# Kernel optimization log

Hardware: AMD Instinct MI355X
Metric: run time of the kernel (lower is better)

## Reference

```python
import jax, jax.numpy as jnp
import numpy as np

N = 50000      # nodes
E = 800000     # edges
IN_DIM = 128
HID = 16       # per-head hidden dim (layer1)
HEADS = 8
OUT_DIM = 32   # layer2 output dim (1 head)
NEG_SLOPE = 0.2  # GAT-paper LeakyReLU slope


def _gat_layer(x, W, a_src, a_dst, src, dst, num_nodes):
    """One multi-head GAT layer.
    x: [N, Fin]; W: [Fin, H*D]; a_src/a_dst: [H, D]; src/dst: [E].
    Returns [N, H, D].
    """
    H, D = a_src.shape
    z = (x @ W).reshape(num_nodes, H, D)            # [N, H, D]
    # edge attention logits: attn_fc([z_src || z_dst]) split into two dots
    e_s = jnp.einsum('nhd,hd->nh', z, a_src)        # [N, H]
    e_d = jnp.einsum('nhd,hd->nh', z, a_dst)        # [N, H]
    e = e_s[src] + e_d[dst]                          # [E, H]
    e = jnp.where(e >= 0, e, NEG_SLOPE * e)          # leaky_relu
    # softmax over incoming edges of each destination node
    m = jax.ops.segment_max(e, dst, num_segments=num_nodes)   # [N, H]
    ex = jnp.exp(e - m[dst])                                   # [E, H]
    s = jax.ops.segment_sum(ex, dst, num_segments=num_nodes)  # [N, H]
    alpha = ex / s[dst]                                        # [E, H]
    msg = alpha[:, :, None] * z[src]                            # [E, H, D]
    return jax.ops.segment_sum(msg, dst, num_segments=num_nodes)  # [N, H, D]


def setup_inputs() -> dict:
    key = jax.random.key(0)
    ks = jax.random.split(key, 9)
    h = jax.random.normal(ks[0], (N, IN_DIM), dtype=jnp.float32)
    src = jax.random.randint(ks[1], (E,), 0, N, dtype=jnp.int32)
    dst = jax.random.randint(ks[2], (E,), 0, N, dtype=jnp.int32)
    sc1 = 1.0 / np.sqrt(IN_DIM)
    W1 = jax.random.normal(ks[3], (IN_DIM, HEADS * HID), dtype=jnp.float32) * sc1
    a1_src = jax.random.normal(ks[4], (HEADS, HID), dtype=jnp.float32) * 0.1
    a1_dst = jax.random.normal(ks[5], (HEADS, HID), dtype=jnp.float32) * 0.1
    sc2 = 1.0 / np.sqrt(HEADS * HID)
    W2 = jax.random.normal(ks[6], (HEADS * HID, OUT_DIM), dtype=jnp.float32) * sc2
    a2_src = jax.random.normal(ks[7], (1, OUT_DIM), dtype=jnp.float32) * 0.1
    a2_dst = jax.random.normal(ks[8], (1, OUT_DIM), dtype=jnp.float32) * 0.1
    return {"h": h, "W1": W1, "a1_src": a1_src, "a1_dst": a1_dst,
            "W2": W2, "a2_src": a2_src, "a2_dst": a2_dst,
            "src": src, "dst": dst}


def reference(h, W1, a1_src, a1_dst, W2, a2_src, a2_dst, src, dst):
    # layer1: multi-head, concat heads -> [N, HEADS*HID]
    h1 = _gat_layer(h, W1, a1_src, a1_dst, src, dst, N).reshape(N, HEADS * HID)
    h1 = jax.nn.elu(h1)
    # layer2: single head -> [N, OUT_DIM]
    out = _gat_layer(h1, W2, a2_src, a2_dst, src, dst, N).reshape(N, OUT_DIM)
    return out
```

## Files before the change

### kernel.cpp

```cpp
#include <hip/hip_runtime.h>
#include <hip/hip_fp16.h>
#include <math.h>

#define NN 50000
#define EE 800000
#define FIN 128
#define F1  128
#define NH  8
#define DH  16
#define F2  32
#define SLOPE 0.2f
#define LOG2E 1.44269504f

#define EB 4096
#define NBLK ((EE + EB - 1) / EB)
#define HB 2048
#define NHBLK ((EE + HB - 1) / HB)
#define BK  391
#define SEGCAP 4096
#define PREPB 80
#define GEMM1B ((NN + 63) / 64)
#define ATT1B  (BK * 8)
#define GEMM2B ((NN + 63) / 64)
#define CHUNK 2560

typedef _Float16 f16x8 __attribute__((ext_vector_type(8)));
typedef float    f32x4 __attribute__((ext_vector_type(4)));

__global__ __launch_bounds__(256) void k1_hist_prep(const int* __restrict__ dst,
        const float* __restrict__ W1, const float* __restrict__ W2,
        __half* __restrict__ wt1, __half* __restrict__ wt2, int* __restrict__ hist) {
    int tid = threadIdx.x;
    if (blockIdx.x < NHBLK) {
        __shared__ int lc[BK];
        for (int i = tid; i < BK; i += 256) lc[i] = 0;
        __syncthreads();
        int base = blockIdx.x * HB;
        int end = base + HB; if (end > EE) end = EE;
        for (int i = base + tid; i < end; i += 256)
            atomicAdd(&lc[dst[i] >> 7], 1);
        __syncthreads();
        for (int i = tid; i < BK; i += 256)
            if (lc[i]) atomicAdd(&hist[i], lc[i]);
    } else {
        int gidx = (blockIdx.x - NHBLK) * 256 + tid;
        if (gidx < FIN * F1) {
            int n = gidx >> 7, k = gidx & 127;
            wt1[gidx] = __float2half(W1[k * F1 + n]);
        } else {
            int t2 = gidx - FIN * F1;
            if (t2 < F2 * FIN) {
                int n = t2 >> 7, k = t2 & 127;
                wt2[t2] = __float2half(W2[k * F2 + n]);
            }
        }
    }
}

extern __shared__ char smem_k2[];
__global__ __launch_bounds__(256) void k2_split_gemm1(const int* __restrict__ src,
        const int* __restrict__ dst, const int* __restrict__ hist, int* __restrict__ cursor,
        unsigned int* __restrict__ sorted,
        const float* __restrict__ h, const __half* __restrict__ wt1,
        const float* __restrict__ a1s, const float* __restrict__ a1d,
        __half* __restrict__ z1s, float* __restrict__ es1x, float* __restrict__ ed1x) {
    int tid = threadIdx.x;
    if (blockIdx.x < NBLK) {
        unsigned int*   recs = (unsigned int*)smem_k2;
        unsigned short* rbk  = (unsigned short*)(smem_k2 + 16384);
        int* lc    = (int*)(smem_k2 + 24576);
        int* lofs  = (int*)(smem_k2 + 26624);
        int* lcur  = (int*)(smem_k2 + 28672);
        int* delta = (int*)(smem_k2 + 30720);
        int* bscan = (int*)(smem_k2 + 32768);
        int* sh    = (int*)(smem_k2 + 34816);
        for (int i = tid; i < 512; i += 256) lc[i] = 0;
        __syncthreads();
        int base = blockIdx.x * EB;
        int cnt = EE - base; if (cnt > EB) cnt = EB;
        unsigned int myrec[16];
        #pragma unroll
        for (int k = 0; k < 16; ++k) {
            int i = base + tid + k * 256;
            myrec[k] = 0xFFFFFFFFu;
            if (i - base < cnt) {
                unsigned int d = (unsigned int)dst[i];
                myrec[k] = (d << 16) | (unsigned int)src[i];
                atomicAdd(&lc[d >> 7], 1);
            }
        }
        __syncthreads();
        int a0 = lc[2 * tid], a1 = lc[2 * tid + 1];
        int tsum = a0 + a1;
        sh[tid] = tsum;
        __syncthreads();
        for (int off = 1; off < 256; off <<= 1) {
            int t = (tid >= off) ? sh[tid - off] : 0;
            __syncthreads(); sh[tid] += t; __syncthreads();
        }
        int ex = sh[tid] - tsum;
        lofs[2 * tid] = ex;
        lofs[2 * tid + 1] = ex + a0;
        __syncthreads();
        int h0 = hist[2 * tid], h1 = hist[2 * tid + 1];
        int hsum = h0 + h1;
        sh[tid] = hsum;
        __syncthreads();
        for (int off = 1; off < 256; off <<= 1) {
            int t = (tid >= off) ? sh[tid - off] : 0;
            __syncthreads(); sh[tid] += t; __syncthreads();
        }
        int hex = sh[tid] - hsum;
        bscan[2 * tid] = hex;
        bscan[2 * tid + 1] = hex + h0;
        __syncthreads();
        for (int b = tid; b < BK; b += 256) {
            int c = lc[b];
            lcur[b] = lofs[b];
            if (c) {
                int g = atomicAdd(&cursor[b], c);
                delta[b] = bscan[b] + g - lofs[b];
            }
        }
        __syncthreads();
        #pragma unroll
        for (int k = 0; k < 16; ++k) {
            if (myrec[k] != 0xFFFFFFFFu) {
                int b = (int)(myrec[k] >> 23);
                int pos = atomicAdd(&lcur[b], 1);
                recs[pos] = myrec[k];
                rbk[pos] = (unsigned short)b;
            }
        }
        __syncthreads();
        for (int s = tid; s < cnt; s += 256)
            sorted[s + delta[rbk[s]]] = recs[s];
    } else {
        __half* hs  = (__half*)smem_k2;
        __half* wls = (__half*)(smem_k2 + 17408);
        for (int c = tid; c < 2048; c += 256) {
            int row = c >> 4, ch = c & 15;
            *(float4*)&wls[row * 136 + ch * 8] = *(const float4*)&wt1[row * 128 + ch * 8];
        }
        int rowBase = (blockIdx.x - NBLK) * 64;
        for (int idx4 = tid; idx4 < 64 * 32; idx4 += 256) {
            int r = idx4 >> 5, cc = (idx4 & 31) * 4;
            int n = rowBase + r;
            float4 v = (n < NN) ? *(const float4*)&h[(size_t)n * FIN + cc] : make_float4(0, 0, 0, 0);
            union { __half2 h2[2]; int2 i; } u;
            u.h2[0] = __floats2half2_rn(v.x, v.y);
            u.h2[1] = __floats2half2_rn(v.z, v.w);
            *(int2*)&hs[r * 136 + cc] = u.i;
        }
        __syncthreads();
        int l = tid & 63, w = tid >> 6;
        int q = l >> 4, cl = l & 15;
        int m0 = w * 16;
        float as[8], ad[8];
        #pragma unroll
        for (int t = 0; t < 8; ++t) { as[t] = a1s[t * DH + cl]; ad[t] = a1d[t * DH + cl]; }
        f32x4 acc[8];
        #pragma unroll
        for (int t = 0; t < 8; ++t) acc[t] = (f32x4){0.f, 0.f, 0.f, 0.f};
        const __half* ap = &hs[(m0 + cl) * 136 + q * 8];
        const __half* bp = &wls[cl * 136 + q * 8];
        #pragma unroll
        for (int k0 = 0; k0 < 128; k0 += 32) {
            f16x8 af = *(const f16x8*)(ap + k0);
            #pragma unroll
            for (int t = 0; t < 8; ++t) {
                f16x8 bf = *(const f16x8*)(bp + t * 16 * 136 + k0);
                acc[t] = __builtin_amdgcn_mfma_f32_16x16x32_f16(af, bf, acc[t], 0, 0, 0);
            }
        }
        #pragma unroll
        for (int t = 0; t < 8; ++t) {
            #pragma unroll
            for (int reg = 0; reg < 4; ++reg) {
                int row = rowBase + m0 + q * 4 + reg;
                float z = acc[t][reg];
                float s = z * as[t], d = z * ad[t];
                s += __shfl_xor(s, 1, 64); d += __shfl_xor(d, 1, 64);
                s += __shfl_xor(s, 2, 64); d += __shfl_xor(d, 2, 64);
                s += __shfl_xor(s, 4, 64); d += __shfl_xor(d, 4, 64);
                s += __shfl_xor(s, 8, 64); d += __shfl_xor(d, 8, 64);
                if (row < NN) {
                    z1s[(size_t)t * (NN * 16) + (size_t)row * 16 + cl] = __float2half(z);
                    if (cl == 0) {
                        es1x[row * NH + t] = s * LOG2E;
                        ed1x[row * NH + t] = d * LOG2E;
                    }
                }
            }
        }
    }
}

__global__ __launch_bounds__(256) void csrbuild_kernel(const int* __restrict__ hist,
        const unsigned int* __restrict__ sorted, unsigned short* __restrict__ csr,
        const float* __restrict__ es1x, const float* __restrict__ ed1x,
        float* __restrict__ w1p, int* __restrict__ row_ptr) {
    __shared__ unsigned int recs[SEGCAP];
    __shared__ unsigned short csr_sh[SEGCAP];
    __shared__ unsigned char dst_sh[SEGCAP];
    __shared__ float ed_sh[128 * NH];
    __shared__ int ncnt[128], ncur[128];
    __shared__ int sh[256];
    __shared__ int bscan[512];
    int b = blockIdx.x;
    int tid = threadIdx.x;
    int h0 = hist[2 * tid], h1 = hist[2 * tid + 1];
    int hsum = h0 + h1;
    sh[tid] = hsum;
    if (tid < 128) ncnt[tid] = 0;
    for (int idx = tid; idx < 128 * NH; idx += 256) {
        int node = b * 128 + (idx >> 3);
        ed_sh[idx] = (node < NN) ? ed1x[node * NH + (idx & 7)] : 0.f;
    }
    __syncthreads();
    for (int off = 1; off < 256; off <<= 1) {
        int t = (tid >= off) ? sh[tid - off] : 0;
        __syncthreads(); sh[tid] += t; __syncthreads();
    }
    int hex = sh[tid] - hsum;
    bscan[2 * tid] = hex;
    bscan[2 * tid + 1] = hex + h0;
    __syncthreads();
    int s0 = bscan[b], s1 = bscan[b + 1];
    int cnt = s1 - s0; if (cnt > SEGCAP) cnt = SEGCAP;
    for (int i = tid; i < cnt; i += 256) {
        unsigned int r = sorted[s0 + i];
        recs[i] = r;
        atomicAdd(&ncnt[(r >> 16) & 127], 1);
    }
    __syncthreads();
    int v = (tid < 128) ? ncnt[tid] : 0;
    sh[tid] = v;
    __syncthreads();
    for (int off = 1; off < 256; off <<= 1) {
        int t = (tid >= off) ? sh[tid - off] : 0;
        __syncthreads(); sh[tid] += t; __syncthreads();
    }
    int ex = sh[tid] - v;
    if (tid < 128) {
        ncur[tid] = ex;
        int node = b * 128 + tid;
        if (node < NN) row_ptr[node] = s0 + ex;
    }
    if (b == BK - 1 && tid == 0) row_ptr[NN] = EE;
    __syncthreads();
    for (int i = tid; i < cnt; i += 256) {
        unsigned int r = recs[i];
        int local = (r >> 16) & 127;
        int p = atomicAdd(&ncur[local], 1);
        csr_sh[p] = (unsigned short)(r & 0xFFFFu);
        dst_sh[p] = (unsigned char)local;
    }
    __syncthreads();
    for (int i = tid; i < cnt; i += 256) {
        unsigned short sv = csr_sh[i];
        unsigned char lv = dst_sh[i];
        csr[s0 + i] = sv;
        float4 ea = *(const float4*)&es1x[(size_t)sv * NH];
        float4 eb = *(const float4*)&es1x[(size_t)sv * NH + 4];
        float es8[8] = {ea.x, ea.y, ea.z, ea.w, eb.x, eb.y, eb.z, eb.w};
        const float* edp = &ed_sh[(int)lv * NH];
        #pragma unroll
        for (int hh = 0; hh < 8; ++hh) {
            float e = es8[hh] + edp[hh];
            e = e >= 0.f ? e : SLOPE * e;
            w1p[(size_t)hh * EE + s0 + i] = exp2f(e);
        }
    }
}

__global__ __launch_bounds__(256, 8) void attn1_slice_kernel(const int* __restrict__ row_ptr,
        const unsigned short* __restrict__ csr, const __half* __restrict__ z1s,
        const float* __restrict__ w1p, __half* __restrict__ h1s) {
    __shared__ unsigned short csr_sh[CHUNK];
    __shared__ float w_sh[CHUNK];
    int hl = blockIdx.x & 7;
    int tile = blockIdx.x >> 3;
    int nodeBase = tile * 128;
    int tid = threadIdx.x;
    int n = nodeBase + (tid >> 1);
    int j = tid & 1;
    const __half* zp = z1s + (size_t)hl * (NN * 16) + j * 8;
    const float* wp = w1p + (size_t)hl * EE;
    int tBeg = row_ptr[nodeBase];
    int nEnd = nodeBase + 128; if (nEnd > NN) nEnd = NN;
    int tEnd = row_ptr[nEnd];
    int b0 = 0, b1 = -1;
    if (n < NN) { b0 = row_ptr[n]; b1 = row_ptr[n + 1]; }
    float acc[8] = {0.f, 0.f, 0.f, 0.f, 0.f, 0.f, 0.f, 0.f};
    float ws = 0.f;
    for (int c0 = tBeg; c0 < tEnd; c0 += CHUNK) {
        int c1 = c0 + CHUNK; if (c1 > tEnd) c1 = tEnd;
        for (int i = c0 + tid; i < c1; i += 256) {
            csr_sh[i - c0] = csr[i];
            w_sh[i - c0] = wp[i];
        }
        __syncthreads();
        int lo = b0 > c0 ? b0 : c0;
        int hi = b1 < c1 ? b1 : c1;
        int i = lo;
        for (; i + 4 <= hi; i += 4) {
            int r = i - c0;
            int s0 = csr_sh[r], s1 = csr_sh[r + 1], s2 = csr_sh[r + 2], s3 = csr_sh[r + 3];
            float w0 = w_sh[r], w1 = w_sh[r + 1], w2 = w_sh[r + 2], w3 = w_sh[r + 3];
            union { float4 f; __half2 h2[4]; } u0, u1, u2, u3;
            u0.f = *(const float4*)&zp[(size_t)s0 * 16];
            u1.f = *(const float4*)&zp[(size_t)s1 * 16];
            u2.f = *(const float4*)&zp[(size_t)s2 * 16];
            u3.f = *(const float4*)&zp[(size_t)s3 * 16];
            ws += (w0 + w1) + (w2 + w3);
            #pragma unroll
            for (int t = 0; t < 4; ++t) {
                float2 v0 = __half22float2(u0.h2[t]);
                float2 v1 = __half22float2(u1.h2[t]);
                float2 v2 = __half22float2(u2.h2[t]);
                float2 v3 = __half22float2(u3.h2[t]);
                acc[2*t]   = fmaf(w0, v0.x, fmaf(w1, v1.x, fmaf(w2, v2.x, fmaf(w3, v3.x, acc[2*t]))));
                acc[2*t+1] = fmaf(w0, v0.y, fmaf(w1, v1.y, fmaf(w2, v2.y, fmaf(w3, v3.y, acc[2*t+1]))));
            }
        }
        for (; i < hi; ++i) {
            int r = i - c0;
            int s = csr_sh[r];
            float wv = w_sh[r];
            ws += wv;
            union { float4 f; __half2 h2[4]; } u;
            u.f = *(const float4*)&zp[(size_t)s * 16];
            #pragma unroll
            for (int t = 0; t < 4; ++t) {
                float2 v = __half22float2(u.h2[t]);
                acc[2*t]   = fmaf(wv, v.x, acc[2*t]);
                acc[2*t+1] = fmaf(wv, v.y, acc[2*t+1]);
            }
        }
        __syncthreads();
    }
    if (n < NN) {
        float rs = ws > 0.f ? 1.0f / ws : 0.f;
        union { float4 f; __half2 h2[4]; } p;
        #pragma unroll
        for (int t = 0; t < 4; ++t) {
            float x0 = acc[2*t] * rs, x1 = acc[2*t+1] * rs;
            x0 = x0 > 0.f ? x0 : __expf(x0) - 1.0f;
            x1 = x1 > 0.f ? x1 : __expf(x1) - 1.0f;
            p.h2[t] = __floats2half2_rn(x0, x1);
        }
        *(float4*)&h1s[(size_t)hl * (NN * 16) + (size_t)n * 16 + j * 8] = p.f;
    }
}

__global__ __launch_bounds__(256) void gemm2_kernel(const __half* __restrict__ h1s,
        const __half* __restrict__ wt2, const float* __restrict__ a2s, const float* __restrict__ a2d,
        __half* __restrict__ z2h, float* __restrict__ es2x, float* __restrict__ ed2x) {
    __shared__ alignas(16) __half hs[64 * 136];
    __shared__ alignas(16) __half wls[32 * 136];
    int tid = threadIdx.x;
    for (int c = tid; c < 512; c += 256) {
        int row = c >> 4, ch = c & 15;
        *(float4*)&wls[row * 136 + ch * 8] = *(const float4*)&wt2[row * 128 + ch * 8];
    }
    int rowBase = blockIdx.x * 64;
    for (int idx = tid; idx < 1024; idx += 256) {
        int j2 = idx & 1, nl = (idx >> 1) & 63, pl = idx >> 7;
        int n = rowBase + nl;
        float4 v = (n < NN) ? *(const float4*)&h1s[(size_t)pl * (NN * 16) + (size_t)n * 16 + j2 * 8]
                            : make_float4(0, 0, 0, 0);
        *(float4*)&hs[nl * 136 + pl * 16 + j2 * 8] = v;
    }
    __syncthreads();
    int l = tid & 63, w = tid >> 6;
    int q = l >> 4, cl = l & 15;
    int m0 = w * 16;
    float as0 = a2s[cl], as1 = a2s[16 + cl];
    float ad0 = a2d[cl], ad1 = a2d[16 + cl];
    f32x4 acc2[2];
    acc2[0] = (f32x4){0.f, 0.f, 0.f, 0.f};
    acc2[1] = (f32x4){0.f, 0.f, 0.f, 0.f};
    const __half* ap = &hs[(m0 + cl) * 136 + q * 8];
    const __half* bp = &wls[cl * 136 + q * 8];
    #pragma unroll
    for (int k0 = 0; k0 < 128; k0 += 32) {
        f16x8 af = *(const f16x8*)(ap + k0);
        #pragma unroll
        for (int t = 0; t < 2; ++t) {
            f16x8 bf = *(const f16x8*)(bp + t * 16 * 136 + k0);
            acc2[t] = __builtin_amdgcn_mfma_f32_16x16x32_f16(af, bf, acc2[t], 0, 0, 0);
        }
    }
    #pragma unroll
    for (int reg = 0; reg < 4; ++reg) {
        int row = rowBase + m0 + q * 4 + reg;
        float s = acc2[0][reg] * as0 + acc2[1][reg] * as1;
        float d = acc2[0][reg] * ad0 + acc2[1][reg] * ad1;
        s += __shfl_xor(s, 1, 64); d += __shfl_xor(d, 1, 64);
        s += __shfl_xor(s, 2, 64); d += __shfl_xor(d, 2, 64);
        s += __shfl_xor(s, 4, 64); d += __shfl_xor(d, 4, 64);
        s += __shfl_xor(s, 8, 64); d += __shfl_xor(d, 8, 64);
        if (row < NN) {
            z2h[(size_t)row * F2 + cl]      = __float2half(acc2[0][reg]);
            z2h[(size_t)row * F2 + 16 + cl] = __float2half(acc2[1][reg]);
            if (cl == 0) {
                es2x[row] = s * LOG2E;
                ed2x[row] = d * LOG2E;
            }
        }
    }
}

__global__ __launch_bounds__(128) void attn2_kernel(const int* __restrict__ row_ptr,
        const unsigned short* __restrict__ csr, const __half* __restrict__ z2h,
        const float* __restrict__ es, const float* __restrict__ ed,
        float* __restrict__ out) {
    int gt = blockIdx.x * 128 + threadIdx.x;
    int n = gt >> 3;
    int j = gt & 7;
    if (n >= NN) return;
    int b0 = row_ptr[n];
    int cnt = row_ptr[n + 1] - b0;
    float edn = ed[n];
    float acc[4] = {0.f, 0.f, 0.f, 0.f};
    float ws = 0.f;
    int i = 0;
    for (; i + 4 <= cnt; i += 4) {
        int s0 = csr[b0 + i], s1 = csr[b0 + i + 1], s2 = csr[b0 + i + 2], s3 = csr[b0 + i + 3];
        float e0 = es[s0] + edn;
        float e1 = es[s1] + edn;
        float e2 = es[s2] + edn;
        float e3 = es[s3] + edn;
        union { float2 f; __half2 h2[2]; } u0, u1, u2, u3;
        u0.f = *(const float2*)&z2h[(size_t)s0 * F2 + j * 4];
        u1.f = *(const float2*)&z2h[(size_t)s1 * F2 + j * 4];
        u2.f = *(const float2*)&z2h[(size_t)s2 * F2 + j * 4];
        u3.f = *(const float2*)&z2h[(size_t)s3 * F2 + j * 4];
        float w0 = exp2f(e0 >= 0.f ? e0 : SLOPE * e0);
        float w1 = exp2f(e1 >= 0.f ? e1 : SLOPE * e1);
        float w2 = exp2f(e2 >= 0.f ? e2 : SLOPE * e2);
        float w3 = exp2f(e3 >= 0.f ? e3 : SLOPE * e3);
        ws += (w0 + w1) + (w2 + w3);
        #pragma unroll
        for (int t = 0; t < 2; ++t) {
            float2 v0 = __half22float2(u0.h2[t]);
            float2 v1 = __half22float2(u1.h2[t]);
            float2 v2 = __half22float2(u2.h2[t]);
            float2 v3 = __half22float2(u3.h2[t]);
            acc[2*t]   = fmaf(w0, v0.x, fmaf(w1, v1.x, fmaf(w2, v2.x, fmaf(w3, v3.x, acc[2*t]))));
            acc[2*t+1] = fmaf(w0, v0.y, fmaf(w1, v1.y, fmaf(w2, v2.y, fmaf(w3, v3.y, acc[2*t+1]))));
        }
    }
    for (; i < cnt; ++i) {
        int s = csr[b0 + i];
        float e = es[s] + edn;
        float wv = exp2f(e >= 0.f ? e : SLOPE * e);
        ws += wv;
        union { float2 f; __half2 h2[2]; } u;
        u.f = *(const float2*)&z2h[(size_t)s * F2 + j * 4];
        #pragma unroll
        for (int t = 0; t < 2; ++t) {
            float2 v = __half22float2(u.h2[t]);
            acc[2*t]   = fmaf(wv, v.x, acc[2*t]);
            acc[2*t+1] = fmaf(wv, v.y, acc[2*t+1]);
        }
    }
    float rs = ws > 0.f ? 1.0f / ws : 0.f;
    *(float4*)&out[(size_t)n * F2 + j * 4] =
        make_float4(acc[0]*rs, acc[1]*rs, acc[2]*rs, acc[3]*rs);
}

extern "C" void kernel_launch(void* const* d_in, const int* in_sizes, int n_in,
                              void* d_out, int out_size, void* d_ws, size_t ws_size,
                              hipStream_t stream) {
    const float* h   = (const float*)d_in[0];
    const float* W1  = (const float*)d_in[1];
    const float* a1s = (const float*)d_in[2];
    const float* a1d = (const float*)d_in[3];
    const float* W2  = (const float*)d_in[4];
    const float* a2s = (const float*)d_in[5];
    const float* a2d = (const float*)d_in[6];
    const int*   src = (const int*)d_in[7];
    const int*   dst = (const int*)d_in[8];
    float* out = (float*)d_out;

    int* ip      = (int*)d_ws;
    int* hist    = ip;
    int* cursor  = hist + 512;
    int* row_ptr = cursor + 512;
    unsigned int* sorted = (unsigned int*)(row_ptr + NN + 8);
    unsigned short* csr16 = (unsigned short*)(sorted + EE);
    float* es1x = (float*)(csr16 + EE);
    float* ed1x = es1x + (size_t)NN * NH;
    float* es2x = ed1x + (size_t)NN * NH;
    float* ed2x = es2x + NN;
    __half* z1s = (__half*)(ed2x + NN);
    __half* z2h = z1s + (size_t)NN * F1;
    __half* wt1 = z2h + (size_t)NN * F2;
    __half* wt2 = wt1 + FIN * F1;
    __half* h1s = wt2 + F2 * FIN;
    float* w1p  = (float*)(h1s + (size_t)NN * F1);

    hipMemsetAsync(hist, 0, 1024 * sizeof(int), stream);

    k1_hist_prep<<<NHBLK + PREPB, 256, 0, stream>>>(dst, W1, W2, wt1, wt2, hist);
    k2_split_gemm1<<<NBLK + GEMM1B, 256, 52224, stream>>>(src, dst, hist, cursor, sorted,
                                                          h, wt1, a1s, a1d, z1s, es1x, ed1x);
    csrbuild_kernel<<<BK, 256, 0, stream>>>(hist, sorted, csr16, es1x, ed1x, w1p, row_ptr);
    attn1_slice_kernel<<<ATT1B, 256, 0, stream>>>(row_ptr, csr16, z1s, w1p, h1s);
    gemm2_kernel<<<GEMM2B, 256, 0, stream>>>(h1s, wt2, a2s, a2d, z2h, es2x, ed2x);
    attn2_kernel<<<(NN * 8 + 127) / 128, 128, 0, stream>>>(row_ptr, csr16, z2h, es2x, ed2x, out);
}
```

Baseline: 200.6 us.

## Stage attn2 edge tiles in shared memory and unroll attn1 gather by eight

attn2 is restructured so each 256-thread block handles 64 nodes: it cooperatively loads the block's contiguous CSR range and the gathered source logits into shared memory, then each thread accumulates two nodes from LDS instead of reading the CSR indices and es values redundantly per 8-lane group. attn1 gains an 8-way unrolled gather loop with occupancy hint lowered from 8 to 4 waves to allow more registers, giving more memory-level parallelism. This costs more register pressure and extra block-wide syncs, and each thread now serially handles two nodes.

```diff
diff --git a/kernel.cpp b/kernel.cpp
--- a/kernel.cpp
+++ b/kernel.cpp
@@ -23,6 +23,8 @@
 #define ATT1B  (BK * 8)
 #define GEMM2B ((NN + 63) / 64)
 #define CHUNK 2560
+#define ATT2B ((NN + 63) / 64)
+#define CHUNK2 1536
 
 typedef _Float16 f16x8 __attribute__((ext_vector_type(8)));
 typedef float    f32x4 __attribute__((ext_vector_type(4)));
@@ -274,7 +276,7 @@
     }
 }
 
-__global__ __launch_bounds__(256, 8) void attn1_slice_kernel(const int* __restrict__ row_ptr,
+__global__ __launch_bounds__(256, 4) void attn1_slice_kernel(const int* __restrict__ row_ptr,
         const unsigned short* __restrict__ csr, const __half* __restrict__ z1s,
         const float* __restrict__ w1p, __half* __restrict__ h1s) {
     __shared__ unsigned short csr_sh[CHUNK];
@@ -304,6 +306,38 @@
         int lo = b0 > c0 ? b0 : c0;
         int hi = b1 < c1 ? b1 : c1;
         int i = lo;
+        for (; i + 8 <= hi; i += 8) {
+            int r = i - c0;
+            int s0 = csr_sh[r],     s1 = csr_sh[r + 1], s2 = csr_sh[r + 2], s3 = csr_sh[r + 3];
+            int s4 = csr_sh[r + 4], s5 = csr_sh[r + 5], s6 = csr_sh[r + 6], s7 = csr_sh[r + 7];
+            float w0 = w_sh[r],     w1 = w_sh[r + 1], w2 = w_sh[r + 2], w3 = w_sh[r + 3];
+            float w4 = w_sh[r + 4], w5 = w_sh[r + 5], w6 = w_sh[r + 6], w7 = w_sh[r + 7];
+            union { float4 f; __half2 h2[4]; } u0, u1, u2, u3, u4, u5, u6, u7;
+            u0.f = *(const float4*)&zp[(size_t)s0 * 16];
+            u1.f = *(const float4*)&zp[(size_t)s1 * 16];
+            u2.f = *(const float4*)&zp[(size_t)s2 * 16];
+            u3.f = *(const float4*)&zp[(size_t)s3 * 16];
+            u4.f = *(const float4*)&zp[(size_t)s4 * 16];
+            u5.f = *(const float4*)&zp[(size_t)s5 * 16];
+            u6.f = *(const float4*)&zp[(size_t)s6 * 16];
+            u7.f = *(const float4*)&zp[(size_t)s7 * 16];
+            ws += ((w0 + w1) + (w2 + w3)) + ((w4 + w5) + (w6 + w7));
+            #pragma unroll
+            for (int t = 0; t < 4; ++t) {
+                float2 v0 = __half22float2(u0.h2[t]);
+                float2 v1 = __half22float2(u1.h2[t]);
+                float2 v2 = __half22float2(u2.h2[t]);
+                float2 v3 = __half22float2(u3.h2[t]);
+                float2 v4 = __half22float2(u4.h2[t]);
+                float2 v5 = __half22float2(u5.h2[t]);
+                float2 v6 = __half22float2(u6.h2[t]);
+                float2 v7 = __half22float2(u7.h2[t]);
+                acc[2*t]   = fmaf(w0, v0.x, fmaf(w1, v1.x, fmaf(w2, v2.x, fmaf(w3, v3.x, acc[2*t]))));
+                acc[2*t]   = fmaf(w4, v4.x, fmaf(w5, v5.x, fmaf(w6, v6.x, fmaf(w7, v7.x, acc[2*t]))));
+                acc[2*t+1] = fmaf(w0, v0.y, fmaf(w1, v1.y, fmaf(w2, v2.y, fmaf(w3, v3.y, acc[2*t+1]))));
+                acc[2*t+1] = fmaf(w4, v4.y, fmaf(w5, v5.y, fmaf(w6, v6.y, fmaf(w7, v7.y, acc[2*t+1]))));
+            }
+        }
         for (; i + 4 <= hi; i += 4) {
             int r = i - c0;
             int s0 = csr_sh[r], s1 = csr_sh[r + 1], s2 = csr_sh[r + 2], s3 = csr_sh[r + 3];
@@ -412,63 +446,98 @@
     }
 }
 
-__global__ __launch_bounds__(128) void attn2_kernel(const int* __restrict__ row_ptr,
+__global__ __launch_bounds__(256) void attn2_kernel(const int* __restrict__ row_ptr,
         const unsigned short* __restrict__ csr, const __half* __restrict__ z2h,
         const float* __restrict__ es, const float* __restrict__ ed,
         float* __restrict__ out) {
-    int gt = blockIdx.x * 128 + threadIdx.x;
-    int n = gt >> 3;
-    int j = gt & 7;
-    if (n >= NN) return;
-    int b0 = row_ptr[n];
-    int cnt = row_ptr[n + 1] - b0;
-    float edn = ed[n];
-    float acc[4] = {0.f, 0.f, 0.f, 0.f};
-    float ws = 0.f;
-    int i = 0;
-    for (; i + 4 <= cnt; i += 4) {
-        int s0 = csr[b0 + i], s1 = csr[b0 + i + 1], s2 = csr[b0 + i + 2], s3 = csr[b0 + i + 3];
-        float e0 = es[s0] + edn;
-        float e1 = es[s1] + edn;
-        float e2 = es[s2] + edn;
-        float e3 = es[s3] + edn;
-        union { float2 f; __half2 h2[2]; } u0, u1, u2, u3;
-        u0.f = *(const float2*)&z2h[(size_t)s0 * F2 + j * 4];
-        u1.f = *(const float2*)&z2h[(size_t)s1 * F2 + j * 4];
-        u2.f = *(const float2*)&z2h[(size_t)s2 * F2 + j * 4];
-        u3.f = *(const float2*)&z2h[(size_t)s3 * F2 + j * 4];
-        float w0 = exp2f(e0 >= 0.f ? e0 : SLOPE * e0);
-        float w1 = exp2f(e1 >= 0.f ? e1 : SLOPE * e1);
-        float w2 = exp2f(e2 >= 0.f ? e2 : SLOPE * e2);
-        float w3 = exp2f(e3 >= 0.f ? e3 : SLOPE * e3);
-        ws += (w0 + w1) + (w2 + w3);
-        #pragma unroll
-        for (int t = 0; t < 2; ++t) {
-            float2 v0 = __half22float2(u0.h2[t]);
-            float2 v1 = __half22float2(u1.h2[t]);
-            float2 v2 = __half22float2(u2.h2[t]);
-            float2 v3 = __half22float2(u3.h2[t]);
-            acc[2*t]   = fmaf(w0, v0.x, fmaf(w1, v1.x, fmaf(w2, v2.x, fmaf(w3, v3.x, acc[2*t]))));
-            acc[2*t+1] = fmaf(w0, v0.y, fmaf(w1, v1.y, fmaf(w2, v2.y, fmaf(w3, v3.y, acc[2*t+1]))));
-        }
-    }
-    for (; i < cnt; ++i) {
-        int s = csr[b0 + i];
-        float e = es[s] + edn;
-        float wv = exp2f(e >= 0.f ? e : SLOPE * e);
-        ws += wv;
-        union { float2 f; __half2 h2[2]; } u;
-        u.f = *(const float2*)&z2h[(size_t)s * F2 + j * 4];
-        #pragma unroll
-        for (int t = 0; t < 2; ++t) {
-            float2 v = __half22float2(u.h2[t]);
-            acc[2*t]   = fmaf(wv, v.x, acc[2*t]);
-            acc[2*t+1] = fmaf(wv, v.y, acc[2*t+1]);
-        }
-    }
-    float rs = ws > 0.f ? 1.0f / ws : 0.f;
-    *(float4*)&out[(size_t)n * F2 + j * 4] =
-        make_float4(acc[0]*rs, acc[1]*rs, acc[2]*rs, acc[3]*rs);
+    __shared__ unsigned short csr_sh[CHUNK2];
+    __shared__ float es_sh[CHUNK2];
+    int nodeBase = blockIdx.x * 64;
+    int tid = threadIdx.x;
+    int j = tid & 7;
+    int na = nodeBase + (tid >> 3);
+    int nb = na + 32;
+    int tBeg = row_ptr[nodeBase];
+    int nEnd = nodeBase + 64; if (nEnd > NN) nEnd = NN;
+    int tEnd = row_ptr[nEnd];
+    int b0a = 0, b1a = -1, b0b = 0, b1b = -1;
+    float edA = 0.f, edB = 0.f;
+    if (na < NN) { b0a = row_ptr[na]; b1a = row_ptr[na + 1]; edA = ed[na]; }
+    if (nb < NN) { b0b = row_ptr[nb]; b1b = row_ptr[nb + 1]; edB = ed[nb]; }
+    float accA[4] = {0.f, 0.f, 0.f, 0.f}, accB[4] = {0.f, 0.f, 0.f, 0.f};
+    float wsA = 0.f, wsB = 0.f;
+    for (int c0 = tBeg; c0 < tEnd; c0 += CHUNK2) {
+        int c1 = c0 + CHUNK2; if (c1 > tEnd) c1 = tEnd;
+        for (int i = c0 + tid; i < c1; i += 256) {
+            unsigned short s = csr[i];
+            csr_sh[i - c0] = s;
+            es_sh[i - c0] = es[s];
+        }
+        __syncthreads();
+        #pragma unroll
+        for (int half = 0; half < 2; ++half) {
+            int lo = (half ? b0b : b0a), hi = (half ? b1b : b1a);
+            float edn = half ? edB : edA;
+            float* acc = half ? accB : accA;
+            float& wsr = half ? wsB : wsA;
+            if (lo < c0) lo = c0;
+            if (hi > c1) hi = c1;
+            int i = lo;
+            for (; i + 4 <= hi; i += 4) {
+                int r = i - c0;
+                int s0 = csr_sh[r], s1 = csr_sh[r + 1], s2 = csr_sh[r + 2], s3 = csr_sh[r + 3];
+                float e0 = es_sh[r] + edn;
+                float e1 = es_sh[r + 1] + edn;
+                float e2 = es_sh[r + 2] + edn;
+                float e3 = es_sh[r + 3] + edn;
+                union { float2 f; __half2 h2[2]; } u0, u1, u2, u3;
+                u0.f = *(const float2*)&z2h[(size_t)s0 * F2 + j * 4];
+                u1.f = *(const float2*)&z2h[(size_t)s1 * F2 + j * 4];
+                u2.f = *(const float2*)&z2h[(size_t)s2 * F2 + j * 4];
+                u3.f = *(const float2*)&z2h[(size_t)s3 * F2 + j * 4];
+                float w0 = exp2f(e0 >= 0.f ? e0 : SLOPE * e0);
+                float w1 = exp2f(e1 >= 0.f ? e1 : SLOPE * e1);
+                float w2 = exp2f(e2 >= 0.f ? e2 : SLOPE * e2);
+                float w3 = exp2f(e3 >= 0.f ? e3 : SLOPE * e3);
+                wsr += (w0 + w1) + (w2 + w3);
+                #pragma unroll
+                for (int t = 0; t < 2; ++t) {
+                    float2 v0 = __half22float2(u0.h2[t]);
+                    float2 v1 = __half22float2(u1.h2[t]);
+                    float2 v2 = __half22float2(u2.h2[t]);
+                    float2 v3 = __half22float2(u3.h2[t]);
+                    acc[2*t]   = fmaf(w0, v0.x, fmaf(w1, v1.x, fmaf(w2, v2.x, fmaf(w3, v3.x, acc[2*t]))));
+                    acc[2*t+1] = fmaf(w0, v0.y, fmaf(w1, v1.y, fmaf(w2, v2.y, fmaf(w3, v3.y, acc[2*t+1]))));
+                }
+            }
+            for (; i < hi; ++i) {
+                int r = i - c0;
+                int s = csr_sh[r];
+                float e = es_sh[r] + edn;
+                float wv = exp2f(e >= 0.f ? e : SLOPE * e);
+                wsr += wv;
+                union { float2 f; __half2 h2[2]; } u;
+                u.f = *(const float2*)&z2h[(size_t)s * F2 + j * 4];
+                #pragma unroll
+                for (int t = 0; t < 2; ++t) {
+                    float2 v = __half22float2(u.h2[t]);
+                    acc[2*t]   = fmaf(wv, v.x, acc[2*t]);
+                    acc[2*t+1] = fmaf(wv, v.y, acc[2*t+1]);
+                }
+            }
+        }
+        __syncthreads();
+    }
+    if (na < NN) {
+        float rs = wsA > 0.f ? 1.0f / wsA : 0.f;
+        *(float4*)&out[(size_t)na * F2 + j * 4] =
+            make_float4(accA[0]*rs, accA[1]*rs, accA[2]*rs, accA[3]*rs);
+    }
+    if (nb < NN) {
+        float rs = wsB > 0.f ? 1.0f / wsB : 0.f;
+        *(float4*)&out[(size_t)nb * F2 + j * 4] =
+            make_float4(accB[0]*rs, accB[1]*rs, accB[2]*rs, accB[3]*rs);
+    }
 }
 
 extern "C" void kernel_launch(void* const* d_in, const int* in_sizes, int n_in,
@@ -510,5 +579,5 @@
     csrbuild_kernel<<<BK, 256, 0, stream>>>(hist, sorted, csr16, es1x, ed1x, w1p, row_ptr);
     attn1_slice_kernel<<<ATT1B, 256, 0, stream>>>(row_ptr, csr16, z1s, w1p, h1s);
     gemm2_kernel<<<GEMM2B, 256, 0, stream>>>(h1s, wt2, a2s, a2d, z2h, es2x, ed2x);
-    attn2_kernel<<<(NN * 8 + 127) / 128, 128, 0, stream>>>(row_ptr, csr16, z2h, es2x, ed2x, out);
-}
+    attn2_kernel<<<ATT2B, 256, 0, stream>>>(row_ptr, csr16, z2h, es2x, ed2x, out);
+}
```

Result: no change. 203.6 us (+1.5%).

## Fold attention vectors into weight GEMMs and tile attn2 per node block

Applied to the files above, without the earlier changes.

Precomputes W·a_src and W·a_dst as extra weight columns, so the MFMA GEMMs emit the edge-logit terms directly and the per-row shuffle reductions go away. This adds one more MFMA tile per GEMM and a little more shared memory. The layer-2 aggregation is rewritten so each block handles 64 nodes: it stages the block's CSR slice and gathered source logits in shared memory in chunks, and each thread covers 8 features with 16-byte loads. Running the logit dot products in fp16 inside the GEMM costs some precision compared with the previous fp32 reductions.

```diff
diff --git a/kernel.cpp b/kernel.cpp
--- a/kernel.cpp
+++ b/kernel.cpp
@@ -18,17 +18,23 @@
 #define NHBLK ((EE + HB - 1) / HB)
 #define BK  391
 #define SEGCAP 4096
-#define PREPB 80
+#define W1XN 144
+#define W2XN 34
+#define PREPB ((W1XN * 128 + W2XN * 128 + 255) / 256)
 #define GEMM1B ((NN + 63) / 64)
 #define ATT1B  (BK * 8)
 #define GEMM2B ((NN + 63) / 64)
 #define CHUNK 2560
+#define ATT2B ((NN + 63) / 64)
+#define CHUNK2 1536
 
 typedef _Float16 f16x8 __attribute__((ext_vector_type(8)));
 typedef float    f32x4 __attribute__((ext_vector_type(4)));
 
 __global__ __launch_bounds__(256) void k1_hist_prep(const int* __restrict__ dst,
         const float* __restrict__ W1, const float* __restrict__ W2,
+        const float* __restrict__ a1s, const float* __restrict__ a1d,
+        const float* __restrict__ a2s, const float* __restrict__ a2d,
         __half* __restrict__ wt1, __half* __restrict__ wt2, int* __restrict__ hist) {
     int tid = threadIdx.x;
     if (blockIdx.x < NHBLK) {
@@ -44,14 +50,38 @@
             if (lc[i]) atomicAdd(&hist[i], lc[i]);
     } else {
         int gidx = (blockIdx.x - NHBLK) * 256 + tid;
-        if (gidx < FIN * F1) {
+        if (gidx < W1XN * 128) {
             int n = gidx >> 7, k = gidx & 127;
-            wt1[gidx] = __float2half(W1[k * F1 + n]);
+            float v;
+            if (n < 128) {
+                v = W1[k * F1 + n];
+            } else if (n < 136) {
+                int c = n - 128; float s = 0.f;
+                #pragma unroll
+                for (int d = 0; d < 16; ++d) s += W1[k * F1 + c * 16 + d] * a1s[c * 16 + d];
+                v = s * LOG2E;
+            } else {
+                int c = n - 136; float s = 0.f;
+                #pragma unroll
+                for (int d = 0; d < 16; ++d) s += W1[k * F1 + c * 16 + d] * a1d[c * 16 + d];
+                v = s * LOG2E;
+            }
+            wt1[gidx] = __float2half(v);
         } else {
-            int t2 = gidx - FIN * F1;
-            if (t2 < F2 * FIN) {
+            int t2 = gidx - W1XN * 128;
+            if (t2 < W2XN * 128) {
                 int n = t2 >> 7, k = t2 & 127;
-                wt2[t2] = __float2half(W2[k * F2 + n]);
+                float v;
+                if (n < 32) {
+                    v = W2[k * F2 + n];
+                } else {
+                    const float* av = (n == 32) ? a2s : a2d;
+                    float s = 0.f;
+                    #pragma unroll
+                    for (int d = 0; d < 32; ++d) s += W2[k * F2 + d] * av[d];
+                    v = s * LOG2E;
+                }
+                wt2[t2] = __float2half(v);
             }
         }
     }
@@ -62,7 +92,6 @@
         const int* __restrict__ dst, const int* __restrict__ hist, int* __restrict__ cursor,
         unsigned int* __restrict__ sorted,
         const float* __restrict__ h, const __half* __restrict__ wt1,
-        const float* __restrict__ a1s, const float* __restrict__ a1d,
         __half* __restrict__ z1s, float* __restrict__ es1x, float* __restrict__ ed1x) {
     int tid = threadIdx.x;
     if (blockIdx.x < NBLK) {
@@ -138,7 +167,7 @@
     } else {
         __half* hs  = (__half*)smem_k2;
         __half* wls = (__half*)(smem_k2 + 17408);
-        for (int c = tid; c < 2048; c += 256) {
+        for (int c = tid; c < W1XN * 16; c += 256) {
             int row = c >> 4, ch = c & 15;
             *(float4*)&wls[row * 136 + ch * 8] = *(const float4*)&wt1[row * 128 + ch * 8];
         }
@@ -156,19 +185,16 @@
         int l = tid & 63, w = tid >> 6;
         int q = l >> 4, cl = l & 15;
         int m0 = w * 16;
-        float as[8], ad[8];
-        #pragma unroll
-        for (int t = 0; t < 8; ++t) { as[t] = a1s[t * DH + cl]; ad[t] = a1d[t * DH + cl]; }
-        f32x4 acc[8];
-        #pragma unroll
-        for (int t = 0; t < 8; ++t) acc[t] = (f32x4){0.f, 0.f, 0.f, 0.f};
+        f32x4 acc[9];
+        #pragma unroll
+        for (int t = 0; t < 9; ++t) acc[t] = (f32x4){0.f, 0.f, 0.f, 0.f};
         const __half* ap = &hs[(m0 + cl) * 136 + q * 8];
         const __half* bp = &wls[cl * 136 + q * 8];
         #pragma unroll
         for (int k0 = 0; k0 < 128; k0 += 32) {
             f16x8 af = *(const f16x8*)(ap + k0);
             #pragma unroll
-            for (int t = 0; t < 8; ++t) {
+            for (int t = 0; t < 9; ++t) {
                 f16x8 bf = *(const f16x8*)(bp + t * 16 * 136 + k0);
                 acc[t] = __builtin_amdgcn_mfma_f32_16x16x32_f16(af, bf, acc[t], 0, 0, 0);
             }
@@ -178,19 +204,17 @@
             #pragma unroll
             for (int reg = 0; reg < 4; ++reg) {
                 int row = rowBase + m0 + q * 4 + reg;
-                float z = acc[t][reg];
-                float s = z * as[t], d = z * ad[t];
-                s += __shfl_xor(s, 1, 64); d += __shfl_xor(d, 1, 64);
-                s += __shfl_xor(s, 2, 64); d += __shfl_xor(d, 2, 64);
-                s += __shfl_xor(s, 4, 64); d += __shfl_xor(d, 4, 64);
-                s += __shfl_xor(s, 8, 64); d += __shfl_xor(d, 8, 64);
-                if (row < NN) {
-                    z1s[(size_t)t * (NN * 16) + (size_t)row * 16 + cl] = __float2half(z);
-                    if (cl == 0) {
-                        es1x[row * NH + t] = s * LOG2E;
-                        ed1x[row * NH + t] = d * LOG2E;
-                    }
-                }
+                if (row < NN)
+                    z1s[(size_t)t * (NN * 16) + (size_t)row * 16 + cl] = __float2half(acc[t][reg]);
+            }
+        }
+        #pragma unroll
+        for (int reg = 0; reg < 4; ++reg) {
+            int row = rowBase + m0 + q * 4 + reg;
+            if (row < NN) {
+                float v = acc[8][reg];
+                if (cl < 8) es1x[row * NH + cl] = v;
+                else        ed1x[row * NH + (cl - 8)] = v;
             }
         }
     }
@@ -355,14 +379,16 @@
 }
 
 __global__ __launch_bounds__(256) void gemm2_kernel(const __half* __restrict__ h1s,
-        const __half* __restrict__ wt2, const float* __restrict__ a2s, const float* __restrict__ a2d,
+        const __half* __restrict__ wt2,
         __half* __restrict__ z2h, float* __restrict__ es2x, float* __restrict__ ed2x) {
     __shared__ alignas(16) __half hs[64 * 136];
-    __shared__ alignas(16) __half wls[32 * 136];
+    __shared__ alignas(16) __half wls[48 * 136];
     int tid = threadIdx.x;
-    for (int c = tid; c < 512; c += 256) {
+    for (int c = tid; c < 48 * 16; c += 256) {
         int row = c >> 4, ch = c & 15;
-        *(float4*)&wls[row * 136 + ch * 8] = *(const float4*)&wt2[row * 128 + ch * 8];
+        float4 v = make_float4(0.f, 0.f, 0.f, 0.f);
+        if (row < W2XN) v = *(const float4*)&wt2[row * 128 + ch * 8];
+        *(float4*)&wls[row * 136 + ch * 8] = v;
     }
     int rowBase = blockIdx.x * 64;
     for (int idx = tid; idx < 1024; idx += 256) {
@@ -376,18 +402,17 @@
     int l = tid & 63, w = tid >> 6;
     int q = l >> 4, cl = l & 15;
     int m0 = w * 16;
-    float as0 = a2s[cl], as1 = a2s[16 + cl];
-    float ad0 = a2d[cl], ad1 = a2d[16 + cl];
-    f32x4 acc2[2];
+    f32x4 acc2[3];
     acc2[0] = (f32x4){0.f, 0.f, 0.f, 0.f};
     acc2[1] = (f32x4){0.f, 0.f, 0.f, 0.f};
+    acc2[2] = (f32x4){0.f, 0.f, 0.f, 0.f};
     const __half* ap = &hs[(m0 + cl) * 136 + q * 8];
     const __half* bp = &wls[cl * 136 + q * 8];
     #pragma unroll
     for (int k0 = 0; k0 < 128; k0 += 32) {
         f16x8 af = *(const f16x8*)(ap + k0);
         #pragma unroll
-        for (int t = 0; t < 2; ++t) {
+        for (int t = 0; t < 3; ++t) {
             f16x8 bf = *(const f16x8*)(bp + t * 16 * 136 + k0);
             acc2[t] = __builtin_amdgcn_mfma_f32_16x16x32_f16(af, bf, acc2[t], 0, 0, 0);
         }
@@ -395,80 +420,95 @@
     #pragma unroll
     for (int reg = 0; reg < 4; ++reg) {
         int row = rowBase + m0 + q * 4 + reg;
-        float s = acc2[0][reg] * as0 + acc2[1][reg] * as1;
-        float d = acc2[0][reg] * ad0 + acc2[1][reg] * ad1;
-        s += __shfl_xor(s, 1, 64); d += __shfl_xor(d, 1, 64);
-        s += __shfl_xor(s, 2, 64); d += __shfl_xor(d, 2, 64);
-        s += __shfl_xor(s, 4, 64); d += __shfl_xor(d, 4, 64);
-        s += __shfl_xor(s, 8, 64); d += __shfl_xor(d, 8, 64);
         if (row < NN) {
             z2h[(size_t)row * F2 + cl]      = __float2half(acc2[0][reg]);
             z2h[(size_t)row * F2 + 16 + cl] = __float2half(acc2[1][reg]);
-            if (cl == 0) {
-                es2x[row] = s * LOG2E;
-                ed2x[row] = d * LOG2E;
-            }
-        }
-    }
-}
-
-__global__ __launch_bounds__(128) void attn2_kernel(const int* __restrict__ row_ptr,
+            if (cl == 0)      es2x[row] = acc2[2][reg];
+            else if (cl == 1) ed2x[row] = acc2[2][reg];
+        }
+    }
+}
+
+__global__ __launch_bounds__(256) void attn2_kernel(const int* __restrict__ row_ptr,
         const unsigned short* __restrict__ csr, const __half* __restrict__ z2h,
         const float* __restrict__ es, const float* __restrict__ ed,
         float* __restrict__ out) {
-    int gt = blockIdx.x * 128 + threadIdx.x;
-    int n = gt >> 3;
-    int j = gt & 7;
-    if (n >= NN) return;
-    int b0 = row_ptr[n];
-    int cnt = row_ptr[n + 1] - b0;
-    float edn = ed[n];
-    float acc[4] = {0.f, 0.f, 0.f, 0.f};
+    __shared__ unsigned short csr_sh[CHUNK2];
+    __shared__ float es_sh[CHUNK2];
+    int nodeBase = blockIdx.x * 64;
+    int tid = threadIdx.x;
+    int j = tid & 3;
+    int n = nodeBase + (tid >> 2);
+    int tBeg = row_ptr[nodeBase];
+    int nEnd = nodeBase + 64; if (nEnd > NN) nEnd = NN;
+    int tEnd = row_ptr[nEnd];
+    int b0 = 0, b1 = -1;
+    float edn = 0.f;
+    if (n < NN) { b0 = row_ptr[n]; b1 = row_ptr[n + 1]; edn = ed[n]; }
+    float acc[8] = {0.f, 0.f, 0.f, 0.f, 0.f, 0.f, 0.f, 0.f};
     float ws = 0.f;
-    int i = 0;
-    for (; i + 4 <= cnt; i += 4) {
-        int s0 = csr[b0 + i], s1 = csr[b0 + i + 1], s2 = csr[b0 + i + 2], s3 = csr[b0 + i + 3];
-        float e0 = es[s0] + edn;
-        float e1 = es[s1] + edn;
-        float e2 = es[s2] + edn;
-        float e3 = es[s3] + edn;
-        union { float2 f; __half2 h2[2]; } u0, u1, u2, u3;
-        u0.f = *(const float2*)&z2h[(size_t)s0 * F2 + j * 4];
-        u1.f = *(const float2*)&z2h[(size_t)s1 * F2 + j * 4];
-        u2.f = *(const float2*)&z2h[(size_t)s2 * F2 + j * 4];
-        u3.f = *(const float2*)&z2h[(size_t)s3 * F2 + j * 4];
-        float w0 = exp2f(e0 >= 0.f ? e0 : SLOPE * e0);
-        float w1 = exp2f(e1 >= 0.f ? e1 : SLOPE * e1);
-        float w2 = exp2f(e2 >= 0.f ? e2 : SLOPE * e2);
-        float w3 = exp2f(e3 >= 0.f ? e3 : SLOPE * e3);
-        ws += (w0 + w1) + (w2 + w3);
-        #pragma unroll
-        for (int t = 0; t < 2; ++t) {
-            float2 v0 = __half22float2(u0.h2[t]);
-            float2 v1 = __half22float2(u1.h2[t]);
-            float2 v2 = __half22float2(u2.h2[t]);
-            float2 v3 = __half22float2(u3.h2[t]);
-            acc[2*t]   = fmaf(w0, v0.x, fmaf(w1, v1.x, fmaf(w2, v2.x, fmaf(w3, v3.x, acc[2*t]))));
-            acc[2*t+1] = fmaf(w0, v0.y, fmaf(w1, v1.y, fmaf(w2, v2.y, fmaf(w3, v3.y, acc[2*t+1]))));
-        }
-    }
-    for (; i < cnt; ++i) {
-        int s = csr[b0 + i];
-        float e = es[s] + edn;
-        float wv = exp2f(e >= 0.f ? e : SLOPE * e);
-        ws += wv;
-        union { float2 f; __half2 h2[2]; } u;
-        u.f = *(const float2*)&z2h[(size_t)s * F2 + j * 4];
-        #pragma unroll
-        for (int t = 0; t < 2; ++t) {
-            float2 v = __half22float2(u.h2[t]);
-            acc[2*t]   = fmaf(wv, v.x, acc[2*t]);
-            acc[2*t+1] = fmaf(wv, v.y, acc[2*t+1]);
-        }
-    }
-    float rs = ws > 0.f ? 1.0f / ws : 0.f;
-    *(float4*)&out[(size_t)n * F2 + j * 4] =
-        make_float4(acc[0]*rs, acc[1]*rs, acc[2]*rs, acc[3]*rs);
+    for (int c0 = tBeg; c0 < tEnd; c0 += CHUNK2) {
+        int c1 = c0 + CHUNK2; if (c1 > tEnd) c1 = tEnd;
+        for (int i = c0 + tid; i < c1; i += 256) {
+            unsigned short s = csr[i];
+            csr_sh[i - c0] = s;
+            es_sh[i - c0] = es[s];
+        }
+        __syncthreads();
+        int lo = b0 > c0 ? b0 : c0;
+        int hi = b1 < c1 ? b1 : c1;
+        int i = lo;
+        for (; i + 4 <= hi; i += 4) {
+            int r = i - c0;
+            int s0 = csr_sh[r], s1 = csr_sh[r + 1], s2 = csr_sh[r + 2], s3 = csr_sh[r + 3];
+            float e0 = es_sh[r] + edn;
+            float e1 = es_sh[r + 1] + edn;
+            float e2 = es_sh[r + 2] + edn;
+            float e3 = es_sh[r + 3] + edn;
+            union { float4 f; __half2 h2[4]; } u0, u1, u2, u3;
+            u0.f = *(const float4*)&z2h[(size_t)s0 * F2 + j * 8];
+            u1.f = *(const float4*)&z2h[(size_t)s1 * F2 + j * 8];
+            u2.f = *(const float4*)&z2h[(size_t)s2 * F2 + j * 8];
+            u3.f = *(const float4*)&z2h[(size_t)s3 * F2 + j * 8];
+            float w0 = exp2f(e0 >= 0.f ? e0 : SLOPE * e0);
+            float w1 = exp2f(e1 >= 0.f ? e1 : SLOPE * e1);
+            float w2 = exp2f(e2 >= 0.f ? e2 : SLOPE * e2);
+            float w3 = exp2f(e3 >= 0.f ? e3 : SLOPE * e3);
+            ws += (w0 + w1) + (w2 + w3);
+            #pragma unroll
+            for (int t = 0; t < 4; ++t) {
+                float2 v0 = __half22float2(u0.h2[t]);
+                float2 v1 = __half22float2(u1.h2[t]);
+                float2 v2 = __half22float2(u2.h2[t]);
+                float2 v3 = __half22float2(u3.h2[t]);
+                acc[2*t]   = fmaf(w0, v0.x, fmaf(w1, v1.x, fmaf(w2, v2.x, fmaf(w3, v3.x, acc[2*t]))));
+                acc[2*t+1] = fmaf(w0, v0.y, fmaf(w1, v1.y, fmaf(w2, v2.y, fmaf(w3, v3.y, acc[2*t+1]))));
+            }
+        }
+        for (; i < hi; ++i) {
+            int r = i - c0;
+            int s = csr_sh[r];
+            float e = es_sh[r] + edn;
+            float wv = exp2f(e >= 0.f ? e : SLOPE * e);
+            ws += wv;
+            union { float4 f; __half2 h2[4]; } u;
+            u.f = *(const float4*)&z2h[(size_t)s * F2 + j * 8];
+            #pragma unroll
+            for (int t = 0; t < 4; ++t) {
+                float2 v = __half22float2(u.h2[t]);
+                acc[2*t]   = fmaf(wv, v.x, acc[2*t]);
+                acc[2*t+1] = fmaf(wv, v.y, acc[2*t+1]);
+            }
+        }
+        __syncthreads();
+    }
+    if (n < NN) {
+        float rs = ws > 0.f ? 1.0f / ws : 0.f;
+        *(float4*)&out[(size_t)n * F2 + j * 8] =
+            make_float4(acc[0]*rs, acc[1]*rs, acc[2]*rs, acc[3]*rs);
+        *(float4*)&out[(size_t)n * F2 + j * 8 + 4] =
+            make_float4(acc[4]*rs, acc[5]*rs, acc[6]*rs, acc[7]*rs);
+    }
 }
 
 extern "C" void kernel_launch(void* const* d_in, const int* in_sizes, int n_in,
@@ -498,17 +538,18 @@
     __half* z1s = (__half*)(ed2x + NN);
     __half* z2h = z1s + (size_t)NN * F1;
     __half* wt1 = z2h + (size_t)NN * F2;
-    __half* wt2 = wt1 + FIN * F1;
-    __half* h1s = wt2 + F2 * FIN;
+    __half* wt2 = wt1 + W1XN * 128;
+    __half* h1s = wt2 + W2XN * 128;
     float* w1p  = (float*)(h1s + (size_t)NN * F1);
 
     hipMemsetAsync(hist, 0, 1024 * sizeof(int), stream);
 
-    k1_hist_prep<<<NHBLK + PREPB, 256, 0, stream>>>(dst, W1, W2, wt1, wt2, hist);
-    k2_split_gemm1<<<NBLK + GEMM1B, 256, 52224, stream>>>(src, dst, hist, cursor, sorted,
-                                                          h, wt1, a1s, a1d, z1s, es1x, ed1x);
+    k1_hist_prep<<<NHBLK + PREPB, 256, 0, stream>>>(dst, W1, W2, a1s, a1d, a2s, a2d,
+                                                    wt1, wt2, hist);
+    k2_split_gemm1<<<NBLK + GEMM1B, 256, 56576, stream>>>(src, dst, hist, cursor, sorted,
+                                                          h, wt1, z1s, es1x, ed1x);
     csrbuild_kernel<<<BK, 256, 0, stream>>>(hist, sorted, csr16, es1x, ed1x, w1p, row_ptr);
     attn1_slice_kernel<<<ATT1B, 256, 0, stream>>>(row_ptr, csr16, z1s, w1p, h1s);
-    gemm2_kernel<<<GEMM2B, 256, 0, stream>>>(h1s, wt2, a2s, a2d, z2h, es2x, ed2x);
-    attn2_kernel<<<(NN * 8 + 127) / 128, 128, 0, stream>>>(row_ptr, csr16, z2h, es2x, ed2x, out);
-}
+    gemm2_kernel<<<GEMM2B, 256, 0, stream>>>(h1s, wt2, z2h, es2x, ed2x);
+    attn2_kernel<<<ATT2B, 256, 0, stream>>>(row_ptr, csr16, z2h, es2x, ed2x, out);
+}
```

After: 193.6 us. 1.04x faster.
